# Optimization experiments

Measured on AMD Instinct MI355X. Metric: run time of the kernel, lower is better.

Reference implementation:

```python
import jax, jax.numpy as jnp
import numpy as np

LRELU = 0.01
EPS = 1e-5
HEADS = 4


def _ln(x, g, b):
    m = x.mean(-1, keepdims=True)
    v = ((x - m) ** 2).mean(-1, keepdims=True)
    return (x - m) / jnp.sqrt(v + EPS) * g + b


def _mapx(x, w1, b1, g1, be1, w2, b2, g2, be2, w3, b3):
    h = jax.nn.leaky_relu(_ln(x @ w1 + b1, g1, be1), LRELU)
    h = jax.nn.leaky_relu(_ln(h @ w2 + b2, g2, be2), LRELU)
    return h @ w3 + b3


def _mcab(x, y, wq, bq, wk, bk, wv, bv, wo, bo, rescale):
    # spectral (channel-wise) multi-head cross attention: q from x, k/v from y
    b, c, h, w = x.shape
    n = h * w
    xt = x.reshape(b, c, n).transpose(0, 2, 1)  # (b, n, c)
    yt = y.reshape(b, c, n).transpose(0, 2, 1)
    dh = c // HEADS
    q = (xt @ wq + bq).reshape(b, n, HEADS, dh).transpose(0, 2, 3, 1)  # (b,H,dh,n)
    k = (yt @ wk + bk).reshape(b, n, HEADS, dh).transpose(0, 2, 3, 1)
    v = (yt @ wv + bv).reshape(b, n, HEADS, dh).transpose(0, 2, 3, 1)
    q = q / (jnp.linalg.norm(q, axis=-1, keepdims=True) + 1e-8)
    k = k / (jnp.linalg.norm(k, axis=-1, keepdims=True) + 1e-8)
    attn = jax.nn.softmax(jnp.einsum('bhdn,bhen->bhde', q, k) * rescale, axis=-1)  # (b,H,dh,dh)
    out = jnp.einsum('bhde,bhen->bhdn', attn, v)  # (b,H,dh,n)
    out = out.transpose(0, 3, 1, 2).reshape(b, n, c) @ wo + bo
    out = out + xt  # residual
    return out.transpose(0, 2, 1).reshape(b, c, h, w)


def setup_inputs() -> dict:
    key = jax.random.key(0)
    ks = jax.random.split(key, 16)
    B, C, H, W, K = 4, 64, 128, 128, 21
    s = 0.02
    nrm = lambda k, shape: jax.random.normal(k, shape, jnp.float32) * s
    return {
        'x': jax.random.normal(ks[0], (B, C, H, W), jnp.float32),
        'semantic': jax.random.uniform(ks[1], (B, K, H, W), jnp.float32),
        'wa': nrm(ks[2], (1, C, 4)), 'ba': jnp.zeros((1, 4), jnp.float32),
        'wb': nrm(ks[3], (20, C, 3)), 'bb': jnp.zeros((20, 3), jnp.float32),
        'in_w': nrm(ks[4], (C, C)), 'in_b': jnp.zeros((C,), jnp.float32),
        'mx_w1': nrm(ks[5], (C, 2 * C)), 'mx_b1': jnp.zeros((2 * C,), jnp.float32),
        'mx_g1': jnp.ones((2 * C,), jnp.float32), 'mx_be1': jnp.zeros((2 * C,), jnp.float32),
        'mx_w2': nrm(ks[6], (2 * C, 2 * C)), 'mx_b2': jnp.zeros((2 * C,), jnp.float32),
        'mx_g2': jnp.ones((2 * C,), jnp.float32), 'mx_be2': jnp.zeros((2 * C,), jnp.float32),
        'mx_w3': nrm(ks[7], (2 * C, C)), 'mx_b3': jnp.zeros((C,), jnp.float32),
        'wq': nrm(ks[8], (C, C)), 'bq': jnp.zeros((C,), jnp.float32),
        'wk': nrm(ks[9], (C, C)), 'bk': jnp.zeros((C,), jnp.float32),
        'wv': nrm(ks[10], (C, C)), 'bv': jnp.zeros((C,), jnp.float32),
        'wo': nrm(ks[11], (C, C)), 'bo': jnp.zeros((C,), jnp.float32),
        'rescale': jnp.ones((HEADS, 1, 1), jnp.float32),
    }


def reference(x, semantic, wa, ba, wb, bb, in_w, in_b,
              mx_w1, mx_b1, mx_g1, mx_be1, mx_w2, mx_b2, mx_g2, mx_be2,
              mx_w3, mx_b3, wq, bq, wk, bk, wv, bv, wo, bo, rescale):
    sem = jax.nn.relu(semantic)            # (b,K,h,w)
    xh = x.transpose(0, 2, 3, 1)           # (b,h,w,c)
    # per-class mask-multiply: (b,K,h,w,c)
    masked = xh[:, None] * sem[:, :, :, :, None]
    # class 0 gets the extra channel (64 = 1*4 + 20*3)
    feat_a = jnp.einsum('bkhwc,kcd->bkhwd', masked[:, :1], wa) + ba[None, :, None, None, :]
    feat_b = jnp.einsum('bkhwc,kcd->bkhwd', masked[:, 1:], wb) + bb[None, :, None, None, :]
    b, _, h, w, _ = feat_a.shape
    feat_a = feat_a.reshape(b, h, w, 4)
    feat_b = jnp.moveaxis(feat_b, 1, 3).reshape(b, h, w, 60)  # preserve class order
    all_feat = jnp.concatenate([feat_a, feat_b], axis=-1)     # (b,h,w,64)
    y = (all_feat @ in_w + in_b).transpose(0, 3, 1, 2)        # (b,c,h,w)
    xm = _mapx(xh, mx_w1, mx_b1, mx_g1, mx_be1, mx_w2, mx_b2, mx_g2, mx_be2, mx_w3, mx_b3)
    xm = xm.transpose(0, 3, 1, 2)
    return _mcab(xm, y, wq, bq, wk, bk, wv, bv, wo, bo, rescale)
```

## Files before the change

kernel.cpp:

```cpp
#include <hip/hip_runtime.h>
#include <hip/hip_bf16.h>

#define NPX 16384
typedef __attribute__((ext_vector_type(8))) short short8;
typedef __attribute__((ext_vector_type(8))) _Float16 half8;
typedef __attribute__((ext_vector_type(4))) _Float16 half4;
typedef __attribute__((ext_vector_type(4))) float f32x4;

#define DEV static __device__ __forceinline__

#define WAB   0
#define WINW  4096
#define W1T   8192
#define W2T   16384
#define W3T   32768
#define WQT   40960
#define WKV   45056
#define WTOT  53248
#define NZERO 4608

DEV float lrelu(float v) { return v >= 0.f ? v : 0.01f * v; }
DEV short f2h(float f) { _Float16 h = (_Float16)f; return __builtin_bit_cast(short, h); }
DEV float h2f(short s) { return (float)__builtin_bit_cast(_Float16, s); }
DEV f32x4 mfmah(half8 a, half8 b, f32x4 c) {
    return __builtin_amdgcn_mfma_f32_16x16x32_f16(a, b, c, 0, 0, 0);
}

template<int K, int NT, int M>
DEV void gemmM(const short* __restrict__ A, int pitch,
               const short* __restrict__ WT, f32x4 (&acc)[M][NT])
{
    int lane = threadIdx.x & 63;
    int ln = lane & 15, q8 = (lane >> 4) * 8;
    const short* bp = WT + ln * K + q8;
    const short* ap = A + (size_t)ln * pitch + q8;
    half8 a[2][M], bb[2][NT];
#pragma unroll
    for (int m = 0; m < M; ++m) a[0][m] = *(const half8*)(ap + m * 16 * pitch);
#pragma unroll
    for (int t = 0; t < NT; ++t) bb[0][t] = *(const half8*)(bp + (size_t)t * 16 * K);
#pragma unroll
    for (int c0 = 0; c0 < K; c0 += 32) {
        const int cur = (c0 >> 5) & 1, nxt = cur ^ 1;
        if (c0 + 32 < K) {
#pragma unroll
            for (int m = 0; m < M; ++m)
                a[nxt][m] = *(const half8*)(ap + m * 16 * pitch + c0 + 32);
#pragma unroll
            for (int t = 0; t < NT; ++t)
                bb[nxt][t] = *(const half8*)(bp + (size_t)t * 16 * K + c0 + 32);
        }
#pragma unroll
        for (int t = 0; t < NT; ++t)
#pragma unroll
            for (int m = 0; m < M; ++m) acc[m][t] = mfmah(a[cur][m], bb[cur][t], acc[m][t]);
    }
}

template<int NT, int M>
DEV void acc_biasM(f32x4 (&acc)[M][NT], const float* __restrict__ bias)
{
    int ln = threadIdx.x & 15;
#pragma unroll
    for (int t = 0; t < NT; ++t) {
        float bv = bias[t * 16 + ln];
        f32x4 v = {bv, bv, bv, bv};
#pragma unroll
        for (int m = 0; m < M; ++m) acc[m][t] = v;
    }
}

template<int NT, int M>
DEV void dstoreM(const f32x4 (&acc)[M][NT], short* sD, int pitch)
{
    int lane = threadIdx.x & 63;
    int ln = lane & 15, r0 = (lane >> 4) * 4;
#pragma unroll
    for (int m = 0; m < M; ++m)
#pragma unroll
        for (int t = 0; t < NT; ++t)
#pragma unroll
            for (int r = 0; r < 4; ++r)
                sD[(m * 16 + r0 + r) * pitch + t * 16 + ln] = f2h(acc[m][t][r]);
}

template<int NT, int M>
DEV void ln_regM(f32x4 (&acc)[M][NT], const float* __restrict__ g, const float* __restrict__ be)
{
    int lane = threadIdx.x & 63, ln = lane & 15;
#pragma unroll
    for (int m = 0; m < M; ++m) {
        f32x4 s = {0,0,0,0}, ss = {0,0,0,0};
#pragma unroll
        for (int t = 0; t < NT; ++t)
#pragma unroll
            for (int r = 0; r < 4; ++r) { float v = acc[m][t][r]; s[r] += v; ss[r] += v * v; }
#pragma unroll
        for (int off = 1; off < 16; off <<= 1)
#pragma unroll
            for (int r = 0; r < 4; ++r) {
                s[r] += __shfl_xor(s[r], off);
                ss[r] += __shfl_xor(ss[r], off);
            }
        f32x4 mm, rs;
#pragma unroll
        for (int r = 0; r < 4; ++r) {
            float mean = s[r] * (1.f / 128.f);
            float var = ss[r] * (1.f / 128.f) - mean * mean;
            mm[r] = mean; rs[r] = rsqrtf(var + 1e-5f);
        }
#pragma unroll
        for (int t = 0; t < NT; ++t) {
            float gg = g[t * 16 + ln], bb = be[t * 16 + ln];
#pragma unroll
            for (int r = 0; r < 4; ++r)
                acc[m][t][r] = lrelu((acc[m][t][r] - mm[r]) * rs[r] * gg + bb);
        }
    }
}

template<int ROWS>
DEV void copyoutR(const short* sD, int pitch, short* __restrict__ dst)
{
    int lane = threadIdx.x & 63;
#pragma unroll
    for (int it = 0; it < ROWS / 8; ++it) {
        int idx = it * 512 + lane * 8;
        int px = idx >> 6, c = idx & 63;
        short8 v = *(const short8*)(&sD[px * pitch + c]);
        *reinterpret_cast<short8*>(dst + (size_t)px * 64 + c) = v;
    }
}

DEV void stage_x16(const float* __restrict__ xb, int n0, short* X)
{
    int lane = threadIdx.x & 63;
    int ln = lane & 15, qd = lane >> 4;
    float vb[16];
#pragma unroll
    for (int t = 0; t < 16; ++t)
        vb[t] = xb[(size_t)(qd * 16 + t) * NPX + n0 + ln];
    short8 lo, hi;
#pragma unroll
    for (int t = 0; t < 8; ++t) { lo[t] = f2h(vb[t]); hi[t] = f2h(vb[8 + t]); }
    *reinterpret_cast<short8*>(&X[ln * 72 + qd * 16]) = lo;
    *reinterpret_cast<short8*>(&X[ln * 72 + qd * 16 + 8]) = hi;
}

__global__ __launch_bounds__(256) void k_prep(const float* __restrict__ wa,
                                              const float* __restrict__ wb,
                                              const float* __restrict__ in_w,
                                              const float* __restrict__ w1,
                                              const float* __restrict__ w2,
                                              const float* __restrict__ w3,
                                              const float* __restrict__ wq,
                                              const float* __restrict__ wk,
                                              const float* __restrict__ wv,
                                              short* __restrict__ wt,
                                              float* __restrict__ gz)
{
    int idx = blockIdx.x * 256 + threadIdx.x;
    if (idx >= WTOT) {
        int z = idx - WTOT;
        if (z < NZERO) gz[z] = 0.f;
        return;
    }
    float v;
    if (idx < WINW) {
        int j = idx >> 6, c = idx & 63;
        v = (j < 4) ? wa[c * 4 + j] : wb[((j - 4) / 3) * 192 + c * 3 + ((j - 4) % 3)];
    } else if (idx < W1T) {
        int i = idx - WINW; v = in_w[(i & 63) * 64 + (i >> 6)];
    } else if (idx < W2T) {
        int i = idx - W1T; v = w1[(i & 63) * 128 + (i >> 6)];
    } else if (idx < W3T) {
        int i = idx - W2T; v = w2[(i & 127) * 128 + (i >> 7)];
    } else if (idx < WQT) {
        int i = idx - W3T; v = w3[(i & 127) * 64 + (i >> 7)];
    } else if (idx < WKV) {
        int i = idx - WQT; v = wq[(i & 63) * 64 + (i >> 6)];
    } else {
        int i = idx - WKV; int e = i >> 6, k = i & 63;
        v = (e < 64) ? wk[k * 64 + e] : wv[k * 64 + (e - 64)];
    }
    wt[idx] = f2h(v);
}

__global__ __launch_bounds__(256, 4) void k_main(const float* __restrict__ x,
                                                 const float* __restrict__ sem,
                                                 const float* __restrict__ ba,
                                                 const float* __restrict__ bbv,
                                                 const float* __restrict__ in_b,
                                                 const float* __restrict__ b1,
                                                 const float* __restrict__ g1,
                                                 const float* __restrict__ be1,
                                                 const float* __restrict__ b2,
                                                 const float* __restrict__ g2,
                                                 const float* __restrict__ be2,
                                                 const float* __restrict__ b3,
                                                 const float* __restrict__ bq,
                                                 const float* __restrict__ bk,
                                                 const float* __restrict__ bv,
                                                 const short* __restrict__ wt,
                                                 short* __restrict__ vout,
                                                 short* __restrict__ xmout,
                                                 float* __restrict__ gram,
                                                 float* __restrict__ nsq)
{
    __shared__ short blob[4][4480];
    int tid = threadIdx.x, w = tid >> 6, lane = tid & 63;
    int ln = lane & 15, qd = lane >> 4, r0 = qd * 4;
    int pw = blockIdx.x * 64 + w * 16;
    int b = pw >> 14, n0 = pw & (NPX - 1);
    const float* xb = x + (size_t)b * 64 * NPX;
    short* X  = blob[w];
    short* T  = blob[w] + 1152;
    short* H  = blob[w] + 2304;
    short* QT = H;
    short* KT = H + 1024;

    stage_x16(xb, n0, X);

    f32x4 acc[1][8];
    acc_biasM<8, 1>(acc, b1);
    gemmM<64, 8, 1>(X, 72, wt + W1T, acc);
    ln_regM<8, 1>(acc, g1, be1);
    dstoreM<8, 1>(acc, H, 136);

    acc_biasM<8, 1>(acc, b2);
    gemmM<128, 8, 1>(H, 136, wt + W2T, acc);
    ln_regM<8, 1>(acc, g2, be2);
    dstoreM<8, 1>(acc, H, 136);

    f32x4 a4[1][4];
    acc_biasM<4, 1>(a4, b3);
    gemmM<128, 4, 1>(H, 136, wt + W3T, a4);
    dstoreM<4, 1>(a4, T, 72);
    copyoutR<16>(T, 72, xmout + (size_t)pw * 64);

    acc_biasM<4, 1>(a4, bq);
    gemmM<64, 4, 1>(T, 72, wt + WQT, a4);
#pragma unroll
    for (int t = 0; t < 4; ++t)
#pragma unroll
        for (int r = 0; r < 4; ++r)
            QT[(t * 16 + ln) * 16 + r0 + r] = f2h(a4[0][t][r]);

    f32x4 a1[1][4];
    { f32x4 z = {0,0,0,0};
      for (int t = 0; t < 4; ++t) a1[0][t] = z; }
    gemmM<64, 4, 1>(X, 72, wt + WAB, a1);
#pragma unroll
    for (int t = 0; t < 4; ++t) {
        int j = t * 16 + ln;
        int cls = (j < 4) ? 0 : 1 + (j - 4) / 3;
        float bias = (j < 4) ? ba[j] : bbv[j - 4];
        f32x4 sm4 = *(const f32x4*)(sem + ((size_t)b * 21 + cls) * NPX + n0 + r0);
#pragma unroll
        for (int r = 0; r < 4; ++r)
            T[(r0 + r) * 72 + j] = f2h(fmaxf(sm4[r], 0.f) * a1[0][t][r] + bias);
    }

    acc_biasM<4, 1>(a4, in_b);
    gemmM<64, 4, 1>(T, 72, wt + WINW, a4);
    dstoreM<4, 1>(a4, X, 72);

    f32x4 a3[1][8];
#pragma unroll
    for (int t = 0; t < 8; ++t) {
        float bvv = (t < 4) ? bk[t * 16 + ln] : bv[(t - 4) * 16 + ln];
        f32x4 vv = {bvv, bvv, bvv, bvv};
        a3[0][t] = vv;
    }
    gemmM<64, 8, 1>(X, 72, wt + WKV, a3);
#pragma unroll
    for (int t = 0; t < 4; ++t)
#pragma unroll
        for (int r = 0; r < 4; ++r)
            KT[(t * 16 + ln) * 16 + r0 + r] = f2h(a3[0][t][r]);
#pragma unroll
    for (int t = 4; t < 8; ++t)
#pragma unroll
        for (int r = 0; r < 4; ++r)
            vout[(size_t)(pw + r0 + r) * 64 + (t - 4) * 16 + ln] = f2h(a3[0][t][r]);

    float* scr = (float*)blob[w];
#pragma unroll
    for (int h = 0; h < 4; ++h) {
        half4 qa = *(const half4*)(&QT[(h * 16 + ln) * 16 + r0]);
        half4 ka = *(const half4*)(&KT[(h * 16 + ln) * 16 + r0]);
        half8 qa8 = {0, 0, 0, 0, 0, 0, 0, 0};
        half8 ka8 = {0, 0, 0, 0, 0, 0, 0, 0};
#pragma unroll
        for (int r = 0; r < 4; ++r) { qa8[r] = qa[r]; ka8[r] = ka[r]; }
        f32x4 z = {0, 0, 0, 0};
        f32x4 aqk = mfmah(qa8, ka8, z);
        f32x4 aqq = mfmah(qa8, qa8, z);
        f32x4 akk = mfmah(ka8, ka8, z);
#pragma unroll
        for (int r = 0; r < 4; ++r) {
            int d = r0 + r;
            scr[h * 256 + d * 16 + ln] = aqk[r];
            if (ln == d) {
                scr[1024 + h * 16 + d] = aqq[r];
                scr[1088 + h * 16 + d] = akk[r];
            }
        }
    }
    __syncthreads();
#pragma unroll
    for (int i = 0; i < 4; ++i) {
        int idx = i * 256 + tid;
        float s = 0.f;
#pragma unroll
        for (int ww = 0; ww < 4; ++ww) s += ((const float*)blob[ww])[idx];
        atomicAdd(&gram[(size_t)b * 1024 + idx], s);
    }
    if (tid < 128) {
        float s = 0.f;
#pragma unroll
        for (int ww = 0; ww < 4; ++ww) s += ((const float*)blob[ww])[1024 + tid];
        atomicAdd(&nsq[(tid >> 6) * 256 + b * 64 + (tid & 63)], s);
    }
}

__global__ __launch_bounds__(256) void k_attnM(const float* __restrict__ gram,
                                               const float* __restrict__ nsq,
                                               const float* __restrict__ rescale,
                                               const float* __restrict__ wo,
                                               short* __restrict__ MT)
{
    __shared__ float s_at[1024];
    int b = blockIdx.x, tid = threadIdx.x;
    if (tid < 64) {
        int h = tid >> 4, d = tid & 15;
        float nq = sqrtf(nsq[b * 64 + h * 16 + d]) + 1e-8f;
        float rsc = rescale[h];
        float lg[16];
#pragma unroll
        for (int e = 0; e < 16; ++e) {
            float nk = sqrtf(nsq[256 + b * 64 + h * 16 + e]) + 1e-8f;
            lg[e] = rsc * gram[b * 1024 + h * 256 + d * 16 + e] / (nq * nk);
        }
        float m = lg[0];
#pragma unroll
        for (int e = 1; e < 16; ++e) m = fmaxf(m, lg[e]);
        float ssum = 0.f;
#pragma unroll
        for (int e = 0; e < 16; ++e) { lg[e] = expf(lg[e] - m); ssum += lg[e]; }
        float inv = 1.f / ssum;
#pragma unroll
        for (int e = 0; e < 16; ++e) s_at[h * 256 + d * 16 + e] = lg[e] * inv;
    }
    __syncthreads();
    int he = tid >> 2, h = he >> 4, e = he & 15;
    int cc0 = (tid & 3) * 16;
#pragma unroll
    for (int cx = 0; cx < 16; ++cx) {
        int cc = cc0 + cx;
        float s = 0.f;
#pragma unroll
        for (int d = 0; d < 16; ++d)
            s = fmaf(s_at[h * 256 + d * 16 + e], wo[(h * 16 + d) * 64 + cc], s);
        MT[b * 4096 + cc * 64 + he] = f2h(s);
    }
}

__global__ __launch_bounds__(256) void k_out(const short* __restrict__ v,
                                             const short* __restrict__ xm,
                                             const short* __restrict__ MT,
                                             const float* __restrict__ bo,
                                             float* __restrict__ out)
{
    int tid = threadIdx.x, w = tid >> 6, lane = tid & 63;
    int ln = lane & 15, qd = lane >> 4;
    int pw = blockIdx.x * 64 + w * 16;
    int b = pw >> 14, n0 = pw & (NPX - 1);

    f32x4 acc[1][4];
    acc_biasM<4, 1>(acc, bo);
    gemmM<64, 4, 1>(v + (size_t)pw * 64, 64, MT + b * 4096, acc);

#pragma unroll
    for (int t = 0; t < 4; ++t) {
        int c = t * 16 + ln;
        f32x4 o;
#pragma unroll
        for (int r = 0; r < 4; ++r)
            o[r] = acc[0][t][r] + h2f(xm[(size_t)(pw + qd * 4 + r) * 64 + c]);
        *reinterpret_cast<f32x4*>(out + ((size_t)b * 64 + c) * NPX + n0 + qd * 4) = o;
    }
}

extern "C" void kernel_launch(void* const* d_in, const int* in_sizes, int n_in,
                              void* d_out, int out_size, void* d_ws, size_t ws_size,
                              hipStream_t stream)
{
    const float* x    = (const float*)d_in[0];
    const float* sem  = (const float*)d_in[1];
    const float* wa   = (const float*)d_in[2];
    const float* ba   = (const float*)d_in[3];
    const float* wb   = (const float*)d_in[4];
    const float* bbv  = (const float*)d_in[5];
    const float* in_w = (const float*)d_in[6];
    const float* in_b = (const float*)d_in[7];
    const float* w1   = (const float*)d_in[8];
    const float* b1   = (const float*)d_in[9];
    const float* g1   = (const float*)d_in[10];
    const float* be1  = (const float*)d_in[11];
    const float* w2   = (const float*)d_in[12];
    const float* b2   = (const float*)d_in[13];
    const float* g2   = (const float*)d_in[14];
    const float* be2  = (const float*)d_in[15];
    const float* w3   = (const float*)d_in[16];
    const float* b3   = (const float*)d_in[17];
    const float* wq   = (const float*)d_in[18];
    const float* bq   = (const float*)d_in[19];
    const float* wk   = (const float*)d_in[20];
    const float* bk   = (const float*)d_in[21];
    const float* wv   = (const float*)d_in[22];
    const float* bv   = (const float*)d_in[23];
    const float* wo   = (const float*)d_in[24];
    const float* bo   = (const float*)d_in[25];
    const float* rescale = (const float*)d_in[26];

    char* wsb = (char*)d_ws;
    short* wt   = (short*)wsb;
    short* vpx  = (short*)(wsb + (1u << 20));
    short* xmp  = (short*)(wsb + (1u << 20) + (8u << 20));
    float* gram = (float*)(wsb + (1u << 20) + (16u << 20));
    float* nsq  = gram + 4096;
    short* MT   = (short*)(nsq + 512);

    dim3 blk(256);
    k_prep<<<dim3(226), blk, 0, stream>>>(wa, wb, in_w, w1, w2, w3, wq, wk, wv, wt, gram);
    k_main<<<dim3(1024), blk, 0, stream>>>(x, sem, ba, bbv, in_b,
                                           b1, g1, be1, b2, g2, be2, b3, bq, bk, bv,
                                           wt, vpx, xmp, gram, nsq);
    k_attnM<<<dim3(4), blk, 0, stream>>>(gram, nsq, rescale, wo, MT);
    k_out<<<dim3(1024), blk, 0, stream>>>(vpx, xmp, MT, bo, (float*)d_out);
}
```

Before: 200.9 us.

## Split fused kernel waves into MLP and semantic/KV roles over 32-pixel tiles

Restructures the main fused kernel so each pair of waves shares a 32-pixel tile. One wave runs the mapx MLP chain and the Q projection while the other runs the semantic mask, input projection and K/V projection, coordinated through shared memory and block barriers. Each wave now processes two 16-row M tiles, so every weight fragment loaded is reused across two MFMAs. The GEMM helper drops its explicit double-buffered register prefetch in favour of simple per-step loads. This adds block-wide syncs and load imbalance between the two roles, and may raise register pressure.

```diff
diff --git a/kernel.cpp b/kernel.cpp
--- a/kernel.cpp
+++ b/kernel.cpp
@@ -34,26 +34,18 @@
     int ln = lane & 15, q8 = (lane >> 4) * 8;
     const short* bp = WT + ln * K + q8;
     const short* ap = A + (size_t)ln * pitch + q8;
-    half8 a[2][M], bb[2][NT];
-#pragma unroll
-    for (int m = 0; m < M; ++m) a[0][m] = *(const half8*)(ap + m * 16 * pitch);
-#pragma unroll
-    for (int t = 0; t < NT; ++t) bb[0][t] = *(const half8*)(bp + (size_t)t * 16 * K);
 #pragma unroll
     for (int c0 = 0; c0 < K; c0 += 32) {
-        const int cur = (c0 >> 5) & 1, nxt = cur ^ 1;
-        if (c0 + 32 < K) {
-#pragma unroll
-            for (int m = 0; m < M; ++m)
-                a[nxt][m] = *(const half8*)(ap + m * 16 * pitch + c0 + 32);
-#pragma unroll
-            for (int t = 0; t < NT; ++t)
-                bb[nxt][t] = *(const half8*)(bp + (size_t)t * 16 * K + c0 + 32);
-        }
-#pragma unroll
-        for (int t = 0; t < NT; ++t)
-#pragma unroll
-            for (int m = 0; m < M; ++m) acc[m][t] = mfmah(a[cur][m], bb[cur][t], acc[m][t]);
+        half8 a[M];
+#pragma unroll
+        for (int m = 0; m < M; ++m)
+            a[m] = *(const half8*)(ap + m * 16 * pitch + c0);
+#pragma unroll
+        for (int t = 0; t < NT; ++t) {
+            half8 b = *(const half8*)(bp + (size_t)t * 16 * K + c0);
+#pragma unroll
+            for (int m = 0; m < M; ++m) acc[m][t] = mfmah(a[m], b, acc[m][t]);
+        }
     }
 }
 
@@ -130,21 +122,6 @@
         short8 v = *(const short8*)(&sD[px * pitch + c]);
         *reinterpret_cast<short8*>(dst + (size_t)px * 64 + c) = v;
     }
-}
-
-DEV void stage_x16(const float* __restrict__ xb, int n0, short* X)
-{
-    int lane = threadIdx.x & 63;
-    int ln = lane & 15, qd = lane >> 4;
-    float vb[16];
-#pragma unroll
-    for (int t = 0; t < 16; ++t)
-        vb[t] = xb[(size_t)(qd * 16 + t) * NPX + n0 + ln];
-    short8 lo, hi;
-#pragma unroll
-    for (int t = 0; t < 8; ++t) { lo[t] = f2h(vb[t]); hi[t] = f2h(vb[8 + t]); }
-    *reinterpret_cast<short8*>(&X[ln * 72 + qd * 16]) = lo;
-    *reinterpret_cast<short8*>(&X[ln * 72 + qd * 16 + 8]) = hi;
 }
 
 __global__ __launch_bounds__(256) void k_prep(const float* __restrict__ wa,
@@ -207,120 +184,157 @@
                                                  float* __restrict__ gram,
                                                  float* __restrict__ nsq)
 {
-    __shared__ short blob[4][4480];
-    int tid = threadIdx.x, w = tid >> 6, lane = tid & 63;
-    int ln = lane & 15, qd = lane >> 4, r0 = qd * 4;
-    int pw = blockIdx.x * 64 + w * 16;
-    int b = pw >> 14, n0 = pw & (NPX - 1);
+    __shared__ short blob[2][8960];
+    const int tid = threadIdx.x, w = tid >> 6, lane = tid & 63;
+    const int ln = lane & 15, qd = lane >> 4, r0 = qd * 4;
+    const int g = w & 1, role = w >> 1;
+    const int pw = blockIdx.x * 64 + g * 32;
+    const int b = pw >> 14, n0 = pw & (NPX - 1);
     const float* xb = x + (size_t)b * 64 * NPX;
-    short* X  = blob[w];
-    short* T  = blob[w] + 1152;
-    short* H  = blob[w] + 2304;
-    short* QT = H;
-    short* KT = H + 1024;
-
-    stage_x16(xb, n0, X);
-
-    f32x4 acc[1][8];
-    acc_biasM<8, 1>(acc, b1);
-    gemmM<64, 8, 1>(X, 72, wt + W1T, acc);
-    ln_regM<8, 1>(acc, g1, be1);
-    dstoreM<8, 1>(acc, H, 136);
-
-    acc_biasM<8, 1>(acc, b2);
-    gemmM<128, 8, 1>(H, 136, wt + W2T, acc);
-    ln_regM<8, 1>(acc, g2, be2);
-    dstoreM<8, 1>(acc, H, 136);
-
-    f32x4 a4[1][4];
-    acc_biasM<4, 1>(a4, b3);
-    gemmM<128, 4, 1>(H, 136, wt + W3T, a4);
-    dstoreM<4, 1>(a4, T, 72);
-    copyoutR<16>(T, 72, xmout + (size_t)pw * 64);
-
-    acc_biasM<4, 1>(a4, bq);
-    gemmM<64, 4, 1>(T, 72, wt + WQT, a4);
-#pragma unroll
-    for (int t = 0; t < 4; ++t)
-#pragma unroll
-        for (int r = 0; r < 4; ++r)
-            QT[(t * 16 + ln) * 16 + r0 + r] = f2h(a4[0][t][r]);
-
-    f32x4 a1[1][4];
-    { f32x4 z = {0,0,0,0};
-      for (int t = 0; t < 4; ++t) a1[0][t] = z; }
-    gemmM<64, 4, 1>(X, 72, wt + WAB, a1);
-#pragma unroll
-    for (int t = 0; t < 4; ++t) {
-        int j = t * 16 + ln;
-        int cls = (j < 4) ? 0 : 1 + (j - 4) / 3;
-        float bias = (j < 4) ? ba[j] : bbv[j - 4];
-        f32x4 sm4 = *(const f32x4*)(sem + ((size_t)b * 21 + cls) * NPX + n0 + r0);
-#pragma unroll
-        for (int r = 0; r < 4; ++r)
-            T[(r0 + r) * 72 + j] = f2h(fmaxf(sm4[r], 0.f) * a1[0][t][r] + bias);
-    }
-
-    acc_biasM<4, 1>(a4, in_b);
-    gemmM<64, 4, 1>(T, 72, wt + WINW, a4);
-    dstoreM<4, 1>(a4, X, 72);
-
-    f32x4 a3[1][8];
-#pragma unroll
-    for (int t = 0; t < 8; ++t) {
-        float bvv = (t < 4) ? bk[t * 16 + ln] : bv[(t - 4) * 16 + ln];
-        f32x4 vv = {bvv, bvv, bvv, bvv};
-        a3[0][t] = vv;
-    }
-    gemmM<64, 8, 1>(X, 72, wt + WKV, a3);
-#pragma unroll
-    for (int t = 0; t < 4; ++t)
-#pragma unroll
-        for (int r = 0; r < 4; ++r)
-            KT[(t * 16 + ln) * 16 + r0 + r] = f2h(a3[0][t][r]);
-#pragma unroll
-    for (int t = 4; t < 8; ++t)
-#pragma unroll
-        for (int r = 0; r < 4; ++r)
-            vout[(size_t)(pw + r0 + r) * 64 + (t - 4) * 16 + ln] = f2h(a3[0][t][r]);
-
-    float* scr = (float*)blob[w];
-#pragma unroll
-    for (int h = 0; h < 4; ++h) {
-        half4 qa = *(const half4*)(&QT[(h * 16 + ln) * 16 + r0]);
-        half4 ka = *(const half4*)(&KT[(h * 16 + ln) * 16 + r0]);
-        half8 qa8 = {0, 0, 0, 0, 0, 0, 0, 0};
-        half8 ka8 = {0, 0, 0, 0, 0, 0, 0, 0};
-#pragma unroll
-        for (int r = 0; r < 4; ++r) { qa8[r] = qa[r]; ka8[r] = ka[r]; }
-        f32x4 z = {0, 0, 0, 0};
-        f32x4 aqk = mfmah(qa8, ka8, z);
-        f32x4 aqq = mfmah(qa8, qa8, z);
-        f32x4 akk = mfmah(ka8, ka8, z);
-#pragma unroll
-        for (int r = 0; r < 4; ++r) {
-            int d = r0 + r;
-            scr[h * 256 + d * 16 + ln] = aqk[r];
-            if (ln == d) {
-                scr[1024 + h * 16 + d] = aqq[r];
-                scr[1088 + h * 16 + d] = akk[r];
+    short* X  = blob[g];
+    short* T  = blob[g] + 2304;
+    short* H  = blob[g] + 4608;
+    short* KT = X;
+    float* scr = (float*)T;
+
+    {
+        float vb[16];
+#pragma unroll
+        for (int t = 0; t < 16; ++t)
+            vb[t] = xb[(size_t)(qd * 16 + t) * NPX + n0 + role * 16 + ln];
+        short8 lo, hi;
+#pragma unroll
+        for (int t = 0; t < 8; ++t) { lo[t] = f2h(vb[t]); hi[t] = f2h(vb[8 + t]); }
+        *reinterpret_cast<short8*>(&X[(role * 16 + ln) * 72 + qd * 16]) = lo;
+        *reinterpret_cast<short8*>(&X[(role * 16 + ln) * 72 + qd * 16 + 8]) = hi;
+    }
+    __syncthreads();
+
+    f32x4 acc8[2][8];
+    if (role == 0) {
+        acc_biasM<8, 2>(acc8, b1);
+        gemmM<64, 8, 2>(X, 72, wt + W1T, acc8);
+    } else {
+        f32x4 a1f[2][4];
+        {
+            f32x4 z = {0,0,0,0};
+#pragma unroll
+            for (int m = 0; m < 2; ++m)
+#pragma unroll
+                for (int t = 0; t < 4; ++t) a1f[m][t] = z;
+        }
+        gemmM<64, 4, 2>(X, 72, wt + WAB, a1f);
+#pragma unroll
+        for (int t = 0; t < 4; ++t) {
+            int j = t * 16 + ln;
+            int cls = (j < 4) ? 0 : 1 + (j - 4) / 3;
+            float bias = (j < 4) ? ba[j] : bbv[j - 4];
+#pragma unroll
+            for (int m = 0; m < 2; ++m) {
+                f32x4 sm4 = *(const f32x4*)(sem + ((size_t)b * 21 + cls) * NPX + n0 + m * 16 + r0);
+#pragma unroll
+                for (int r = 0; r < 4; ++r)
+                    T[(m * 16 + r0 + r) * 72 + j] = f2h(fmaxf(sm4[r], 0.f) * a1f[m][t][r] + bias);
             }
         }
     }
     __syncthreads();
+
+    f32x4 aqreg[2][4];
+    if (role == 0) {
+        ln_regM<8, 2>(acc8, g1, be1);
+        dstoreM<8, 2>(acc8, H, 136);
+        acc_biasM<8, 2>(acc8, b2);
+        gemmM<128, 8, 2>(H, 136, wt + W2T, acc8);
+        ln_regM<8, 2>(acc8, g2, be2);
+        dstoreM<8, 2>(acc8, H, 136);
+        f32x4 a4[2][4];
+        acc_biasM<4, 2>(a4, b3);
+        gemmM<128, 4, 2>(H, 136, wt + W3T, a4);
+        dstoreM<4, 2>(a4, H, 72);
+        copyoutR<32>(H, 72, xmout + (size_t)pw * 64);
+        acc_biasM<4, 2>(aqreg, bq);
+        gemmM<64, 4, 2>(H, 72, wt + WQT, aqreg);
+    } else {
+        f32x4 a4[2][4];
+        acc_biasM<4, 2>(a4, in_b);
+        gemmM<64, 4, 2>(T, 72, wt + WINW, a4);
+        dstoreM<4, 2>(a4, T, 72);
+        f32x4 a3[2][8];
+#pragma unroll
+        for (int t = 0; t < 8; ++t) {
+            float bvv = (t < 4) ? bk[t * 16 + ln] : bv[(t - 4) * 16 + ln];
+            f32x4 vv = {bvv, bvv, bvv, bvv};
+            a3[0][t] = vv; a3[1][t] = vv;
+        }
+        gemmM<64, 8, 2>(T, 72, wt + WKV, a3);
+#pragma unroll
+        for (int h = 0; h < 4; ++h) {
+            f32x4 akk = {0, 0, 0, 0};
+#pragma unroll
+            for (int m = 0; m < 2; ++m) {
+                half8 ka8 = {0, 0, 0, 0, 0, 0, 0, 0};
+#pragma unroll
+                for (int r = 0; r < 4; ++r) {
+                    short hv = f2h(a3[m][h][r]);
+                    KT[(h * 16 + ln) * 32 + m * 16 + r0 + r] = hv;
+                    ka8[r] = __builtin_bit_cast(_Float16, hv);
+                }
+                akk = mfmah(ka8, ka8, akk);
+            }
+#pragma unroll
+            for (int r = 0; r < 4; ++r)
+                if (ln == r0 + r) scr[h * 16 + r0 + r] = akk[r];
+        }
+#pragma unroll
+        for (int t = 4; t < 8; ++t)
+#pragma unroll
+            for (int m = 0; m < 2; ++m)
+#pragma unroll
+                for (int r = 0; r < 4; ++r)
+                    vout[(size_t)(pw + m * 16 + r0 + r) * 64 + (t - 4) * 16 + ln] = f2h(a3[m][t][r]);
+    }
+    __syncthreads();
+
+    if (role == 0) {
+#pragma unroll
+        for (int h = 0; h < 4; ++h) {
+            f32x4 aqk = {0,0,0,0}, aqq = {0,0,0,0};
+#pragma unroll
+            for (int m = 0; m < 2; ++m) {
+                half4 kv4 = *(const half4*)(&KT[(h * 16 + ln) * 32 + m * 16 + r0]);
+                half8 qa8 = {0, 0, 0, 0, 0, 0, 0, 0};
+                half8 ka8 = {0, 0, 0, 0, 0, 0, 0, 0};
+#pragma unroll
+                for (int r = 0; r < 4; ++r) {
+                    qa8[r] = (_Float16)aqreg[m][h][r];
+                    ka8[r] = kv4[r];
+                }
+                aqk = mfmah(qa8, ka8, aqk);
+                aqq = mfmah(qa8, qa8, aqq);
+            }
+#pragma unroll
+            for (int r = 0; r < 4; ++r) {
+                int d = r0 + r;
+                scr[64 + h * 256 + d * 16 + ln] = aqk[r];
+                if (ln == d) scr[1088 + h * 16 + d] = aqq[r];
+            }
+        }
+    }
+    __syncthreads();
+
+    const float* s0 = (const float*)(blob[0] + 2304);
+    const float* s1 = (const float*)(blob[1] + 2304);
 #pragma unroll
     for (int i = 0; i < 4; ++i) {
         int idx = i * 256 + tid;
-        float s = 0.f;
-#pragma unroll
-        for (int ww = 0; ww < 4; ++ww) s += ((const float*)blob[ww])[idx];
-        atomicAdd(&gram[(size_t)b * 1024 + idx], s);
-    }
-    if (tid < 128) {
-        float s = 0.f;
-#pragma unroll
-        for (int ww = 0; ww < 4; ++ww) s += ((const float*)blob[ww])[1024 + tid];
-        atomicAdd(&nsq[(tid >> 6) * 256 + b * 64 + (tid & 63)], s);
+        atomicAdd(&gram[(size_t)b * 1024 + idx], s0[64 + idx] + s1[64 + idx]);
+    }
+    if (tid < 64) {
+        atomicAdd(&nsq[b * 64 + tid], s0[1088 + tid] + s1[1088 + tid]);
+    } else if (tid < 128) {
+        int t2 = tid - 64;
+        atomicAdd(&nsq[256 + b * 64 + t2], s0[t2] + s1[t2]);
     }
 }
 
```

Result: faster. 178.9 us (-10.9%).
